# Kernel tuning notes

Hardware: AMD Instinct MI355X
Metric: run time of the kernel (lower is better)

Reference implementation:

```python
import jax, jax.numpy as jnp
import numpy as np

OUT, IN = 11008, 4096  # weight matrix shape (out_features, in_features)
TOKENS = 64


def setup_inputs() -> dict:
    key = jax.random.key(0)
    k1, k2, k3 = jax.random.split(key, 3)
    x = jax.random.normal(k1, (TOKENS, IN), dtype=jnp.float32)
    # packed 1-bit weights: each int holds 8 sign bits (values 0..255)
    bp = jax.random.randint(k2, (OUT * IN // 8,), 0, 256, dtype=jnp.int32)
    # per-output-row scale, broadcasts over bit_mat rows
    scale = jax.random.uniform(k3, (OUT, 1), dtype=jnp.float32) * 0.02 + 0.001
    return {"x": x, "bp": bp, "scale": scale}


def _unpack_bits(bp):
    # bp: [N] ints in [0,256). Extract bits MSB-first (i=0 -> bit 7), map {0,1}->{-1,+1}.
    shifts = jnp.arange(7, -1, -1, dtype=jnp.int32)  # [8]
    bits = (bp[:, None] >> shifts) & 1               # [N, 8]
    return (bits.reshape(-1) * 2 - 1)                # [N*8] in {-1, +1}


def reference(x, bp, scale):
    bit_mat = _unpack_bits(bp).reshape(OUT, IN).astype(x.dtype)  # [OUT, IN]
    w = bit_mat * scale                                          # [OUT, IN]
    return x @ w.T                                               # [TOKENS, OUT]
```

## Files before the change

### kernel.cpp

```cpp
#include <hip/hip_runtime.h>
#include <stdint.h>

using short8 = __attribute__((ext_vector_type(8))) short;
using f32x4  = __attribute__((ext_vector_type(4))) float;

#define OUT_F 11008
#define IN_F  4096
#define TOK   64
#define WPR   (IN_F/8)
#define BN    128
#define KSPLIT 4
#define KQ    (IN_F/KSPLIT)
#define BK    256
#define NCH   (KQ/BK)
#define NBLK  (OUT_F/BN)

__device__ __forceinline__ unsigned short f2bf(float f) {
    uint32_t u = __float_as_uint(f);
    u += 0x7FFFu + ((u >> 16) & 1u);
    return (unsigned short)(u >> 16);
}

__global__ __launch_bounds__(256) void cvt_kernel(const float* __restrict__ x,
                                                  unsigned short* __restrict__ xb) {
    int t = blockIdx.x * 256 + threadIdx.x;
    const float4* xv = (const float4*)x;
    float4 a = xv[2*t], b = xv[2*t+1];
    union { short8 v; unsigned short u[8]; } o;
    o.u[0]=f2bf(a.x); o.u[1]=f2bf(a.y); o.u[2]=f2bf(a.z); o.u[3]=f2bf(a.w);
    o.u[4]=f2bf(b.x); o.u[5]=f2bf(b.y); o.u[6]=f2bf(b.z); o.u[7]=f2bf(b.w);
    ((short8*)xb)[t] = o.v;
}

__device__ __forceinline__ short8 unpack_w(uint32_t w) {
    union { short8 v; uint32_t u[4]; } r;
#pragma unroll
    for (int p = 0; p < 4; ++p) {
        uint32_t lo = (w << (8  + 2*p)) & 0x8000u;
        uint32_t hi = (w << (25 + 2*p)) & 0x80000000u;
        r.u[p] = 0xBF80BF80u ^ lo ^ hi;
    }
    return r.v;
}

__global__ __launch_bounds__(256) void gemm_kernel(const unsigned short* __restrict__ xb,
                                                   const uint32_t* __restrict__ bp,
                                                   const float* __restrict__ scale,
                                                   float* __restrict__ out) {
    __shared__ __align__(128) unsigned char xs[TOK * BK * 2];

    const int bid  = blockIdx.x;
    const int nblk = bid % NBLK;
    const int q    = bid / NBLK;
    const int n0   = nblk * BN;
    const int tid  = threadIdx.x;
    const int wv   = tid >> 6;
    const int lane = tid & 63;
    const int l15  = lane & 15;
    const int lg   = lane >> 4;

    f32x4 acc[2][4];
#pragma unroll
    for (int nf = 0; nf < 2; ++nf)
#pragma unroll
        for (int mt = 0; mt < 4; ++mt) acc[nf][mt] = (f32x4){0.f, 0.f, 0.f, 0.f};

    const int nr0 = n0 + wv*32 + l15;
    const uint32_t* bpr0 = bp + (size_t)nr0 * WPR + q*(KQ/8) + lg;
    const uint32_t* bpr1 = bpr0 + 16*WPR;

    const int srow   = tid >> 5;
    const int scolsw = ((tid & 31) * 16) ^ ((srow & 7) << 4);
    const unsigned char* xbb = (const unsigned char*)xb;

    for (int c = 0; c < NCH; ++c) {
        __syncthreads();
        const int kcb = (q*KQ + c*BK) * 2;
#pragma unroll
        for (int i = 0; i < 8; ++i) {
            int row = i*8 + srow;
            const void* g = xbb + row*(IN_F*2) + kcb + scolsw;
            void* l = (void*)(xs + i*4096 + wv*1024);
            __builtin_amdgcn_global_load_lds(
                (const __attribute__((address_space(1))) void*)g,
                (__attribute__((address_space(3))) void*)l,
                16, 0, 0);
        }
        __syncthreads();

        const int wbase = c*(BK/8);
#pragma unroll
        for (int kk = 0; kk < 8; ++kk) {
            uint32_t w0 = bpr0[wbase + kk*4];
            uint32_t w1 = bpr1[wbase + kk*4];
            short8 b0 = unpack_w(w0);
            short8 b1 = unpack_w(w1);
#pragma unroll
            for (int mt = 0; mt < 4; ++mt) {
                int row = mt*16 + l15;
                int ba  = (row*512 + kk*64 + lg*16) ^ ((row & 7) << 4);
                short8 af = *(const short8*)(xs + ba);
                acc[0][mt] = __builtin_amdgcn_mfma_f32_16x16x32_bf16(af, b0, acc[0][mt], 0, 0, 0);
                acc[1][mt] = __builtin_amdgcn_mfma_f32_16x16x32_bf16(af, b1, acc[1][mt], 0, 0, 0);
            }
        }
    }

    float sc0 = scale[n0 + wv*32 + l15];
    float sc1 = scale[n0 + wv*32 + 16 + l15];
#pragma unroll
    for (int mt = 0; mt < 4; ++mt)
#pragma unroll
        for (int j = 0; j < 4; ++j) {
            int m = mt*16 + lg*4 + j;
            atomicAdd(out + (size_t)m*OUT_F + n0 + wv*32 + l15,      acc[0][mt][j]*sc0);
            atomicAdd(out + (size_t)m*OUT_F + n0 + wv*32 + 16 + l15, acc[1][mt][j]*sc1);
        }
}

extern "C" void kernel_launch(void* const* d_in, const int* in_sizes, int n_in,
                              void* d_out, int out_size, void* d_ws, size_t ws_size,
                              hipStream_t stream) {
    const float*    x     = (const float*)d_in[0];
    const uint32_t* bp    = (const uint32_t*)d_in[1];
    const float*    scale = (const float*)d_in[2];
    float* out = (float*)d_out;
    unsigned short* xb = (unsigned short*)d_ws;

    hipMemsetAsync(d_out, 0, (size_t)TOK * OUT_F * sizeof(float), stream);
    cvt_kernel<<<dim3((TOK*IN_F)/(256*8)), dim3(256), 0, stream>>>(x, xb);
    gemm_kernel<<<dim3(NBLK*KSPLIT), dim3(256), 0, stream>>>(xb, bp, scale, out);
}
```

Baseline: 95.02 us.

## Fuse x conversion into GEMM, prefetch weights, replace atomics with split-K reduce

Drops the separate fp32-to-bf16 conversion kernel and converts x while staging it into LDS inside the GEMM. All packed weight words for the block's K slice are loaded into registers up front, so their latency overlaps the first LDS fill. Split-K goes from 4 to 8 slices, and the atomicAdd epilogue plus memset are replaced by plain stores into per-slice partial buffers followed by a separate reduce kernel. In exchange, each block now reads fp32 x directly (twice the bytes, with no async global-to-LDS copy), uses more registers, and writes and re-reads about 22 MB of partials.

```diff
diff --git a/kernel.cpp b/kernel.cpp
--- a/kernel.cpp
+++ b/kernel.cpp
@@ -9,27 +9,17 @@
 #define TOK   64
 #define WPR   (IN_F/8)
 #define BN    128
-#define KSPLIT 4
+#define KSPLIT 8
 #define KQ    (IN_F/KSPLIT)
 #define BK    256
 #define NCH   (KQ/BK)
 #define NBLK  (OUT_F/BN)
+#define PARTF (TOK*OUT_F)
 
 __device__ __forceinline__ unsigned short f2bf(float f) {
     uint32_t u = __float_as_uint(f);
     u += 0x7FFFu + ((u >> 16) & 1u);
     return (unsigned short)(u >> 16);
-}
-
-__global__ __launch_bounds__(256) void cvt_kernel(const float* __restrict__ x,
-                                                  unsigned short* __restrict__ xb) {
-    int t = blockIdx.x * 256 + threadIdx.x;
-    const float4* xv = (const float4*)x;
-    float4 a = xv[2*t], b = xv[2*t+1];
-    union { short8 v; unsigned short u[8]; } o;
-    o.u[0]=f2bf(a.x); o.u[1]=f2bf(a.y); o.u[2]=f2bf(a.z); o.u[3]=f2bf(a.w);
-    o.u[4]=f2bf(b.x); o.u[5]=f2bf(b.y); o.u[6]=f2bf(b.z); o.u[7]=f2bf(b.w);
-    ((short8*)xb)[t] = o.v;
 }
 
 __device__ __forceinline__ short8 unpack_w(uint32_t w) {
@@ -43,10 +33,10 @@
     return r.v;
 }
 
-__global__ __launch_bounds__(256) void gemm_kernel(const unsigned short* __restrict__ xb,
+__global__ __launch_bounds__(256) void gemm_kernel(const float* __restrict__ x,
                                                    const uint32_t* __restrict__ bp,
                                                    const float* __restrict__ scale,
-                                                   float* __restrict__ out) {
+                                                   float* __restrict__ pw) {
     __shared__ __align__(128) unsigned char xs[TOK * BK * 2];
 
     const int bid  = blockIdx.x;
@@ -59,42 +49,45 @@
     const int l15  = lane & 15;
     const int lg   = lane >> 4;
 
+    const uint32_t* b0p = bp + (size_t)(n0 + wv*32 + l15) * WPR + q*(KQ/8) + lg;
+    const uint32_t* b1p = b0p + 16 * WPR;
+    uint32_t wA[NCH][8], wB[NCH][8];
+#pragma unroll
+    for (int c = 0; c < NCH; ++c)
+#pragma unroll
+        for (int kk = 0; kk < 8; ++kk) {
+            wA[c][kk] = b0p[c*32 + kk*4];
+            wB[c][kk] = b1p[c*32 + kk*4];
+        }
+    const float sc0 = scale[n0 + wv*32 + l15];
+    const float sc1 = scale[n0 + wv*32 + 16 + l15];
+
     f32x4 acc[2][4];
 #pragma unroll
     for (int nf = 0; nf < 2; ++nf)
 #pragma unroll
         for (int mt = 0; mt < 4; ++mt) acc[nf][mt] = (f32x4){0.f, 0.f, 0.f, 0.f};
 
-    const int nr0 = n0 + wv*32 + l15;
-    const uint32_t* bpr0 = bp + (size_t)nr0 * WPR + q*(KQ/8) + lg;
-    const uint32_t* bpr1 = bpr0 + 16*WPR;
-
-    const int srow   = tid >> 5;
-    const int scolsw = ((tid & 31) * 16) ^ ((srow & 7) << 4);
-    const unsigned char* xbb = (const unsigned char*)xb;
-
     for (int c = 0; c < NCH; ++c) {
-        __syncthreads();
-        const int kcb = (q*KQ + c*BK) * 2;
+        if (c) __syncthreads();
+        const float* xc = x + q*KQ + c*BK;
 #pragma unroll
-        for (int i = 0; i < 8; ++i) {
-            int row = i*8 + srow;
-            const void* g = xbb + row*(IN_F*2) + kcb + scolsw;
-            void* l = (void*)(xs + i*4096 + wv*1024);
-            __builtin_amdgcn_global_load_lds(
-                (const __attribute__((address_space(1))) void*)g,
-                (__attribute__((address_space(3))) void*)l,
-                16, 0, 0);
+        for (int it = 0; it < 16; ++it) {
+            int f  = tid + it*256;
+            int r  = f >> 6;
+            int c4 = f & 63;
+            float4 v = *(const float4*)(xc + (size_t)r*IN_F + c4*4);
+            uint32_t lo = (uint32_t)f2bf(v.x) | ((uint32_t)f2bf(v.y) << 16);
+            uint32_t hi = (uint32_t)f2bf(v.z) | ((uint32_t)f2bf(v.w) << 16);
+            int a = (r*512 + c4*8) ^ ((r & 7) << 4);
+            *(uint2*)(xs + a) = make_uint2(lo, hi);
         }
         __syncthreads();
 
-        const int wbase = c*(BK/8);
 #pragma unroll
         for (int kk = 0; kk < 8; ++kk) {
-            uint32_t w0 = bpr0[wbase + kk*4];
-            uint32_t w1 = bpr1[wbase + kk*4];
-            short8 b0 = unpack_w(w0);
-            short8 b1 = unpack_w(w1);
+            short8 b0 = unpack_w(wA[c][kk]);
+            short8 b1 = unpack_w(wB[c][kk]);
 #pragma unroll
             for (int mt = 0; mt < 4; ++mt) {
                 int row = mt*16 + l15;
@@ -106,16 +99,27 @@
         }
     }
 
-    float sc0 = scale[n0 + wv*32 + l15];
-    float sc1 = scale[n0 + wv*32 + 16 + l15];
+    float* base = pw + (size_t)q * PARTF;
 #pragma unroll
     for (int mt = 0; mt < 4; ++mt)
 #pragma unroll
         for (int j = 0; j < 4; ++j) {
             int m = mt*16 + lg*4 + j;
-            atomicAdd(out + (size_t)m*OUT_F + n0 + wv*32 + l15,      acc[0][mt][j]*sc0);
-            atomicAdd(out + (size_t)m*OUT_F + n0 + wv*32 + 16 + l15, acc[1][mt][j]*sc1);
+            base[(size_t)m*OUT_F + n0 + wv*32 + l15]      = acc[0][mt][j]*sc0;
+            base[(size_t)m*OUT_F + n0 + wv*32 + 16 + l15] = acc[1][mt][j]*sc1;
         }
+}
+
+__global__ __launch_bounds__(256) void reduce_kernel(const float4* __restrict__ pw,
+                                                     float4* __restrict__ out) {
+    int i = blockIdx.x * 256 + threadIdx.x;
+    float4 s = pw[i];
+#pragma unroll
+    for (int qq = 1; qq < KSPLIT; ++qq) {
+        float4 t = pw[(size_t)qq*(PARTF/4) + i];
+        s.x += t.x; s.y += t.y; s.z += t.z; s.w += t.w;
+    }
+    out[i] = s;
 }
 
 extern "C" void kernel_launch(void* const* d_in, const int* in_sizes, int n_in,
@@ -124,10 +128,9 @@
     const float*    x     = (const float*)d_in[0];
     const uint32_t* bp    = (const uint32_t*)d_in[1];
     const float*    scale = (const float*)d_in[2];
-    float* out = (float*)d_out;
-    unsigned short* xb = (unsigned short*)d_ws;
+    float* pw = (float*)d_ws;
 
-    hipMemsetAsync(d_out, 0, (size_t)TOK * OUT_F * sizeof(float), stream);
-    cvt_kernel<<<dim3((TOK*IN_F)/(256*8)), dim3(256), 0, stream>>>(x, xb);
-    gemm_kernel<<<dim3(NBLK*KSPLIT), dim3(256), 0, stream>>>(xb, bp, scale, out);
+    gemm_kernel<<<dim3(NBLK*KSPLIT), dim3(256), 0, stream>>>(x, bp, scale, pw);
+    reduce_kernel<<<dim3((PARTF/4)/256), dim3(256), 0, stream>>>((const float4*)pw,
+                                                                 (float4*)d_out);
 }
```

Result: slower. 100.9 us (+6.1%).
